# Performance work log

Hardware: AMD Instinct MI355X
Metric: run time of the kernel (lower is better)

## Reference

```python
import jax, jax.numpy as jnp
import numpy as np

VOCAB, D, PAD, SPARSITY = 6, 32, 5, 0.15


def setup_inputs() -> dict:
    key = jax.random.key(0)
    ks = jax.random.split(key, 16)
    x = jax.random.randint(ks[0], (256, 4096), 0, VOCAB, dtype=jnp.int32)
    s = 0.1
    emb = jax.random.normal(ks[1], (VOCAB, D), jnp.float32) * s
    return {
        "x": x,
        "emb": emb,
        # selector: D -> D//2 -> 1 (sigmoid)
        "sel_w1": jax.random.normal(ks[2], (D, D // 2), jnp.float32) * s,
        "sel_b1": jnp.zeros((D // 2,), jnp.float32),
        "sel_w2": jax.random.normal(ks[3], (D // 2, 1), jnp.float32) * s,
        "sel_b2": jnp.zeros((1,), jnp.float32),
        # approximator: D -> D -> D
        "app_w1": jax.random.normal(ks[4], (D, D), jnp.float32) * s,
        "app_b1": jnp.zeros((D,), jnp.float32),
        "app_w2": jax.random.normal(ks[5], (D, D), jnp.float32) * s,
        "app_b2": jnp.zeros((D,), jnp.float32),
        # classifier: D -> D//2 -> 1 (sigmoid)
        "cls_w1": jax.random.normal(ks[6], (D, D // 2), jnp.float32) * s,
        "cls_b1": jnp.zeros((D // 2,), jnp.float32),
        "cls_w2": jax.random.normal(ks[7], (D // 2, 1), jnp.float32) * s,
        "cls_b2": jnp.zeros((1,), jnp.float32),
    }


def reference(x, emb, sel_w1, sel_b1, sel_w2, sel_b2,
              app_w1, app_b1, app_w2, app_b2,
              cls_w1, cls_b1, cls_w2, cls_b2):
    B, S = x.shape
    k = max(1, int(S * SPARSITY))
    table = emb.at[PAD].set(0.0)            # padding_idx row is zero
    e = table[x]                            # [B, S, D]
    # selector scores (tiny MLP + sigmoid)
    h = jax.nn.relu(e @ sel_w1 + sel_b1)
    scores = jax.nn.sigmoid((h @ sel_w2 + sel_b2).squeeze(-1))  # [B, S]
    _, top_idx = jax.lax.top_k(scores, k)   # [B, k]
    sel = jnp.take_along_axis(e, top_idx[..., None], axis=1)    # [B, k, D]
    a = jax.nn.relu(sel @ app_w1 + app_b1) @ app_w2 + app_b2    # [B, k, D]
    pooled = a.mean(axis=1)                 # [B, D]
    c = jax.nn.relu(pooled @ cls_w1 + cls_b1)
    pred = jax.nn.sigmoid((c @ cls_w2 + cls_b2).squeeze(-1))    # [B]
    return pred, top_idx, scores
```

## Files before the change

### kernel.cpp

```cpp
#include <hip/hip_runtime.h>
#include <math.h>

#define VOCABN 6
#define DIM 32
#define PADI 5
#define BATCH 256
#define SEQ 4096
#define KSEL 614

__global__ __launch_bounds__(256) void fused_row_kernel(
    const int* __restrict__ x,
    const float* __restrict__ emb,
    const float* __restrict__ sel_w1, const float* __restrict__ sel_b1,
    const float* __restrict__ sel_w2, const float* __restrict__ sel_b2,
    const float* __restrict__ app_w1, const float* __restrict__ app_b1,
    const float* __restrict__ app_w2, const float* __restrict__ app_b2,
    const float* __restrict__ cls_w1, const float* __restrict__ cls_b1,
    const float* __restrict__ cls_w2, const float* __restrict__ cls_b2,
    float* __restrict__ out_pred,
    float* __restrict__ out_topidx,
    float* __restrict__ out_scores) {
    const int b = blockIdx.x;
    const int t = threadIdx.x;
    const int lane = t & 63;
    const int w = t >> 6;

    __shared__ float s_emb[VOCABN * DIM];
    __shared__ float s_selw1[DIM * (DIM / 2)];
    __shared__ float s_selb1[DIM / 2], s_selw2[DIM / 2];
    __shared__ float s_appw1[DIM * DIM];
    __shared__ float s_appb1[DIM];
    __shared__ float s_appw2[DIM * DIM];
    __shared__ float s_appb2[DIM];
    __shared__ float s_clsw1[DIM * (DIM / 2)];
    __shared__ float s_clsb1[DIM / 2], s_clsw2[DIM / 2];
    __shared__ float s_selb2, s_clsb2v;
    __shared__ float s_selh[VOCABN * (DIM / 2)];
    __shared__ float s_ah[VOCABN * DIM];
    __shared__ float s_a[VOCABN * DIM];
    __shared__ float s_score[VOCABN];
    __shared__ int s_wtot[4][VOCABN];
    __shared__ int s_sel[VOCABN], s_base[VOCABN];
    __shared__ float s_pooled[DIM], s_c[DIM / 2];

    int tok[16];
    const int4* xp = (const int4*)(x + (size_t)b * SEQ + t * 16);
    int4 tw0 = xp[0], tw1 = xp[1], tw2 = xp[2], tw3 = xp[3];

    if (t < VOCABN * DIM) s_emb[t] = (t >= PADI * DIM) ? 0.f : emb[t];
    for (int i = t; i < 512; i += 256) { s_selw1[i] = sel_w1[i]; s_clsw1[i] = cls_w1[i]; }
    for (int i = t; i < 1024; i += 256) { s_appw1[i] = app_w1[i]; s_appw2[i] = app_w2[i]; }
    if (t < 16) { s_selb1[t] = sel_b1[t]; s_selw2[t] = sel_w2[t];
                  s_clsb1[t] = cls_b1[t]; s_clsw2[t] = cls_w2[t]; }
    if (t < 32) { s_appb1[t] = app_b1[t]; s_appb2[t] = app_b2[t]; }
    if (t == 0) { s_selb2 = sel_b2[0]; s_clsb2v = cls_b2[0]; }

    tok[0] = tw0.x; tok[1] = tw0.y; tok[2] = tw0.z; tok[3] = tw0.w;
    tok[4] = tw1.x; tok[5] = tw1.y; tok[6] = tw1.z; tok[7] = tw1.w;
    tok[8] = tw2.x; tok[9] = tw2.y; tok[10] = tw2.z; tok[11] = tw2.w;
    tok[12] = tw3.x; tok[13] = tw3.y; tok[14] = tw3.z; tok[15] = tw3.w;
    __syncthreads();

    if (t < VOCABN * (DIM / 2)) {
        const int v = t >> 4, j = t & 15;
        float acc = s_selb1[j];
        #pragma unroll
        for (int d = 0; d < DIM; ++d) acc += s_emb[v * DIM + d] * s_selw1[d * (DIM / 2) + j];
        s_selh[t] = fmaxf(acc, 0.f);
    }
    __syncthreads();

    if (t < VOCABN * DIM) {
        const int v = t >> 5, j = t & 31;
        float acc = s_appb1[j];
        #pragma unroll
        for (int d = 0; d < DIM; ++d) acc += s_emb[v * DIM + d] * s_appw1[d * DIM + j];
        s_ah[t] = fmaxf(acc, 0.f);
    } else if (t < VOCABN * DIM + VOCABN) {
        const int v = t - VOCABN * DIM;
        float z = s_selb2;
        #pragma unroll
        for (int j = 0; j < DIM / 2; ++j) z += s_selh[v * (DIM / 2) + j] * s_selw2[j];
        s_score[v] = 1.f / (1.f + expf(-z));
    }
    __syncthreads();

    if (t < VOCABN * DIM) {
        const int v = t >> 5, d = t & 31;
        float acc = s_appb2[d];
        #pragma unroll
        for (int j = 0; j < DIM; ++j) acc += s_ah[v * DIM + j] * s_appw2[j * DIM + d];
        s_a[t] = acc;
    }

    {
        float4* sp = (float4*)(out_scores + (size_t)b * SEQ + t * 16);
        #pragma unroll
        for (int q = 0; q < 4; ++q) {
            float4 f;
            f.x = s_score[tok[q * 4 + 0]];
            f.y = s_score[tok[q * 4 + 1]];
            f.z = s_score[tok[q * 4 + 2]];
            f.w = s_score[tok[q * 4 + 3]];
            sp[q] = f;
        }
    }

    int cnt[VOCABN], val[VOCABN];
    #pragma unroll
    for (int v = 0; v < VOCABN; ++v) {
        int c = 0;
        #pragma unroll
        for (int i = 0; i < 16; ++i) c += (tok[i] == v) ? 1 : 0;
        cnt[v] = c; val[v] = c;
    }
    for (int off = 1; off < 64; off <<= 1) {
        #pragma unroll
        for (int v = 0; v < VOCABN; ++v) {
            int up = __shfl_up(val[v], off, 64);
            if (lane >= off) val[v] += up;
        }
    }
    if (lane == 63) {
        #pragma unroll
        for (int v = 0; v < VOCABN; ++v) s_wtot[w][v] = val[v];
    }
    __syncthreads();

    int excl[VOCABN];
    #pragma unroll
    for (int v = 0; v < VOCABN; ++v) {
        int pre = 0;
        for (int ww = 0; ww < 4; ++ww) pre += (ww < w) ? s_wtot[ww][v] : 0;
        excl[v] = pre + val[v] - cnt[v];
    }

    if (t == 0) {
        int rank[VOCABN];
        #pragma unroll
        for (int v = 0; v < VOCABN; ++v) {
            const float my = s_score[v];
            int r = 0;
            for (int u = 0; u < VOCABN; ++u) {
                if (s_score[u] > my) ++r;
                else if (s_score[u] == my && u < v) ++r;
            }
            rank[r] = v;
        }
        int rem = KSEL;
        for (int r = 0; r < VOCABN; ++r) {
            const int v = rank[r];
            const int tot = s_wtot[0][v] + s_wtot[1][v] + s_wtot[2][v] + s_wtot[3][v];
            const int take = tot < rem ? tot : rem;
            s_base[v] = KSEL - rem;
            s_sel[v] = take;
            rem -= take;
        }
    }
    __syncthreads();

    #pragma unroll
    for (int v = 0; v < VOCABN; ++v) {
        int p = excl[v];
        const int sel = s_sel[v];
        const int bs = s_base[v];
        #pragma unroll
        for (int i = 0; i < 16; ++i) {
            if (tok[i] == v) {
                if (p < sel) out_topidx[(size_t)b * KSEL + bs + p] = (float)(t * 16 + i);
                ++p;
            }
        }
    }

    if (t < DIM) {
        float acc = 0.f;
        #pragma unroll
        for (int v = 0; v < VOCABN; ++v) acc += (float)s_sel[v] * s_a[v * DIM + t];
        s_pooled[t] = acc / (float)KSEL;
    }
    __syncthreads();
    if (t < DIM / 2) {
        float acc = s_clsb1[t];
        #pragma unroll
        for (int d = 0; d < DIM; ++d) acc += s_pooled[d] * s_clsw1[d * (DIM / 2) + t];
        s_c[t] = fmaxf(acc, 0.f);
    }
    __syncthreads();
    if (t == 0) {
        float z = s_clsb2v;
        #pragma unroll
        for (int j = 0; j < DIM / 2; ++j) z += s_c[j] * s_clsw2[j];
        out_pred[b] = 1.f / (1.f + expf(-z));
    }
}

extern "C" void kernel_launch(void* const* d_in, const int* in_sizes, int n_in,
                              void* d_out, int out_size, void* d_ws, size_t ws_size,
                              hipStream_t stream) {
    const int*   x      = (const int*)  d_in[0];
    const float* emb    = (const float*)d_in[1];
    const float* sel_w1 = (const float*)d_in[2];
    const float* sel_b1 = (const float*)d_in[3];
    const float* sel_w2 = (const float*)d_in[4];
    const float* sel_b2 = (const float*)d_in[5];
    const float* app_w1 = (const float*)d_in[6];
    const float* app_b1 = (const float*)d_in[7];
    const float* app_w2 = (const float*)d_in[8];
    const float* app_b2 = (const float*)d_in[9];
    const float* cls_w1 = (const float*)d_in[10];
    const float* cls_b1 = (const float*)d_in[11];
    const float* cls_w2 = (const float*)d_in[12];
    const float* cls_b2 = (const float*)d_in[13];

    float* out = (float*)d_out;
    float* out_pred   = out;
    float* out_topidx = out + BATCH;
    float* out_scores = out + BATCH + BATCH * KSEL;

    fused_row_kernel<<<BATCH, 256, 0, stream>>>(
        x, emb, sel_w1, sel_b1, sel_w2, sel_b2,
        app_w1, app_b1, app_w2, app_b2,
        cls_w1, cls_b1, cls_w2, cls_b2,
        out_pred, out_topidx, out_scores);
}
```

Measured before the change: 91.48 us.

## Use 1024 threads per row and fuse selector MLP into one shuffle-reduced phase

Each row's block grows from 256 to 1024 threads, so every thread handles 4 tokens instead of 16 and the cross-wave scan spans 16 waves. The selector hidden layer and output projection now run in one phase with a warp-shuffle reduction, which removes one barrier and the s_selh buffer. Weight loading is spread across more threads. The trade-off is more waves per block and a longer serial cross-wave prefix and total sum over 16 entries, which could limit occupancy with only 256 blocks.

Result: no change. 90.14 us (-1.5%).

```diff
diff --git a/kernel.cpp b/kernel.cpp
--- a/kernel.cpp
+++ b/kernel.cpp
@@ -8,7 +8,7 @@
 #define SEQ 4096
 #define KSEL 614
 
-__global__ __launch_bounds__(256) void fused_row_kernel(
+__global__ __launch_bounds__(1024) void fused_row_kernel(
     const int* __restrict__ x,
     const float* __restrict__ emb,
     const float* __restrict__ sel_w1, const float* __restrict__ sel_b1,
@@ -35,75 +35,65 @@
     __shared__ float s_clsw1[DIM * (DIM / 2)];
     __shared__ float s_clsb1[DIM / 2], s_clsw2[DIM / 2];
     __shared__ float s_selb2, s_clsb2v;
-    __shared__ float s_selh[VOCABN * (DIM / 2)];
     __shared__ float s_ah[VOCABN * DIM];
     __shared__ float s_a[VOCABN * DIM];
     __shared__ float s_score[VOCABN];
-    __shared__ int s_wtot[4][VOCABN];
+    __shared__ int s_wtot[16][VOCABN];
     __shared__ int s_sel[VOCABN], s_base[VOCABN];
     __shared__ float s_pooled[DIM], s_c[DIM / 2];
 
-    int tok[16];
-    const int4* xp = (const int4*)(x + (size_t)b * SEQ + t * 16);
-    int4 tw0 = xp[0], tw1 = xp[1], tw2 = xp[2], tw3 = xp[3];
+    const int4 tw = *(const int4*)(x + (size_t)b * SEQ + t * 4);
 
     if (t < VOCABN * DIM) s_emb[t] = (t >= PADI * DIM) ? 0.f : emb[t];
-    for (int i = t; i < 512; i += 256) { s_selw1[i] = sel_w1[i]; s_clsw1[i] = cls_w1[i]; }
-    for (int i = t; i < 1024; i += 256) { s_appw1[i] = app_w1[i]; s_appw2[i] = app_w2[i]; }
-    if (t < 16) { s_selb1[t] = sel_b1[t]; s_selw2[t] = sel_w2[t];
-                  s_clsb1[t] = cls_b1[t]; s_clsw2[t] = cls_w2[t]; }
-    if (t < 32) { s_appb1[t] = app_b1[t]; s_appb2[t] = app_b2[t]; }
-    if (t == 0) { s_selb2 = sel_b2[0]; s_clsb2v = cls_b2[0]; }
-
-    tok[0] = tw0.x; tok[1] = tw0.y; tok[2] = tw0.z; tok[3] = tw0.w;
-    tok[4] = tw1.x; tok[5] = tw1.y; tok[6] = tw1.z; tok[7] = tw1.w;
-    tok[8] = tw2.x; tok[9] = tw2.y; tok[10] = tw2.z; tok[11] = tw2.w;
-    tok[12] = tw3.x; tok[13] = tw3.y; tok[14] = tw3.z; tok[15] = tw3.w;
-    __syncthreads();
-
-    if (t < VOCABN * (DIM / 2)) {
-        const int v = t >> 4, j = t & 15;
-        float acc = s_selb1[j];
-        #pragma unroll
-        for (int d = 0; d < DIM; ++d) acc += s_emb[v * DIM + d] * s_selw1[d * (DIM / 2) + j];
-        s_selh[t] = fmaxf(acc, 0.f);
-    }
-    __syncthreads();
-
-    if (t < VOCABN * DIM) {
-        const int v = t >> 5, j = t & 31;
+    if (t < 512) s_selw1[t] = sel_w1[t];
+    else if (t < 1024) s_clsw1[t - 512] = cls_w1[t - 512];
+    s_appw1[t] = app_w1[t];
+    s_appw2[t] = app_w2[t];
+    if (t >= 192 && t < 208) { int i = t - 192; s_selb1[i] = sel_b1[i]; s_selw2[i] = sel_w2[i]; }
+    else if (t >= 208 && t < 224) { int i = t - 208; s_clsb1[i] = cls_b1[i]; s_clsw2[i] = cls_w2[i]; }
+    else if (t >= 224 && t < 256) { int i = t - 224; s_appb1[i] = app_b1[i]; s_appb2[i] = app_b2[i]; }
+    else if (t == 256) s_selb2 = sel_b2[0];
+    else if (t == 257) s_clsb2v = cls_b2[0];
+
+    int tok[4];
+    tok[0] = tw.x; tok[1] = tw.y; tok[2] = tw.z; tok[3] = tw.w;
+    __syncthreads();
+
+    if (t < 48) {
+        const int v = t >> 3, j0 = (t & 7) * 2;
+        float h0 = s_selb1[j0], h1 = s_selb1[j0 + 1];
+        #pragma unroll
+        for (int d = 0; d < DIM; ++d) {
+            const float e = s_emb[v * DIM + d];
+            h0 += e * s_selw1[d * (DIM / 2) + j0];
+            h1 += e * s_selw1[d * (DIM / 2) + j0 + 1];
+        }
+        float part = fmaxf(h0, 0.f) * s_selw2[j0] + fmaxf(h1, 0.f) * s_selw2[j0 + 1];
+        part += __shfl_xor(part, 1, 64);
+        part += __shfl_xor(part, 2, 64);
+        part += __shfl_xor(part, 4, 64);
+        if ((t & 7) == 0) s_score[v] = 1.f / (1.f + expf(-(part + s_selb2)));
+    } else if (t >= 128 && t < 128 + VOCABN * DIM) {
+        const int i = t - 128, v = i >> 5, j = i & 31;
         float acc = s_appb1[j];
         #pragma unroll
         for (int d = 0; d < DIM; ++d) acc += s_emb[v * DIM + d] * s_appw1[d * DIM + j];
-        s_ah[t] = fmaxf(acc, 0.f);
-    } else if (t < VOCABN * DIM + VOCABN) {
-        const int v = t - VOCABN * DIM;
-        float z = s_selb2;
-        #pragma unroll
-        for (int j = 0; j < DIM / 2; ++j) z += s_selh[v * (DIM / 2) + j] * s_selw2[j];
-        s_score[v] = 1.f / (1.f + expf(-z));
-    }
-    __syncthreads();
-
-    if (t < VOCABN * DIM) {
-        const int v = t >> 5, d = t & 31;
+        s_ah[i] = fmaxf(acc, 0.f);
+    }
+    __syncthreads();
+
+    if (t >= 128 && t < 128 + VOCABN * DIM) {
+        const int i = t - 128, v = i >> 5, d = i & 31;
         float acc = s_appb2[d];
         #pragma unroll
         for (int j = 0; j < DIM; ++j) acc += s_ah[v * DIM + j] * s_appw2[j * DIM + d];
-        s_a[t] = acc;
-    }
-
+        s_a[i] = acc;
+    }
     {
-        float4* sp = (float4*)(out_scores + (size_t)b * SEQ + t * 16);
-        #pragma unroll
-        for (int q = 0; q < 4; ++q) {
-            float4 f;
-            f.x = s_score[tok[q * 4 + 0]];
-            f.y = s_score[tok[q * 4 + 1]];
-            f.z = s_score[tok[q * 4 + 2]];
-            f.w = s_score[tok[q * 4 + 3]];
-            sp[q] = f;
-        }
+        float4 f;
+        f.x = s_score[tok[0]]; f.y = s_score[tok[1]];
+        f.z = s_score[tok[2]]; f.w = s_score[tok[3]];
+        *(float4*)(out_scores + (size_t)b * SEQ + t * 4) = f;
     }
 
     int cnt[VOCABN], val[VOCABN];
@@ -111,7 +101,7 @@
     for (int v = 0; v < VOCABN; ++v) {
         int c = 0;
         #pragma unroll
-        for (int i = 0; i < 16; ++i) c += (tok[i] == v) ? 1 : 0;
+        for (int i = 0; i < 4; ++i) c += (tok[i] == v) ? 1 : 0;
         cnt[v] = c; val[v] = c;
     }
     for (int off = 1; off < 64; off <<= 1) {
@@ -131,7 +121,7 @@
     #pragma unroll
     for (int v = 0; v < VOCABN; ++v) {
         int pre = 0;
-        for (int ww = 0; ww < 4; ++ww) pre += (ww < w) ? s_wtot[ww][v] : 0;
+        for (int ww = 0; ww < w; ++ww) pre += s_wtot[ww][v];
         excl[v] = pre + val[v] - cnt[v];
     }
 
@@ -150,7 +140,8 @@
         int rem = KSEL;
         for (int r = 0; r < VOCABN; ++r) {
             const int v = rank[r];
-            const int tot = s_wtot[0][v] + s_wtot[1][v] + s_wtot[2][v] + s_wtot[3][v];
+            int tot = 0;
+            for (int ww = 0; ww < 16; ++ww) tot += s_wtot[ww][v];
             const int take = tot < rem ? tot : rem;
             s_base[v] = KSEL - rem;
             s_sel[v] = take;
@@ -165,9 +156,9 @@
         const int sel = s_sel[v];
         const int bs = s_base[v];
         #pragma unroll
-        for (int i = 0; i < 16; ++i) {
+        for (int i = 0; i < 4; ++i) {
             if (tok[i] == v) {
-                if (p < sel) out_topidx[(size_t)b * KSEL + bs + p] = (float)(t * 16 + i);
+                if (p < sel) out_topidx[(size_t)b * KSEL + bs + p] = (float)(t * 4 + i);
                 ++p;
             }
         }
@@ -218,7 +209,7 @@
     float* out_topidx = out + BATCH;
     float* out_scores = out + BATCH + BATCH * KSEL;
 
-    fused_row_kernel<<<BATCH, 256, 0, stream>>>(
+    fused_row_kernel<<<BATCH, 1024, 0, stream>>>(
         x, emb, sel_w1, sel_b1, sel_w2, sel_b2,
         app_w1, app_b1, app_w2, app_b2,
         cls_w1, cls_b1, cls_w2, cls_b2,
```
